# Performance work log

Measured on AMD Instinct MI355X. Metric: run time of the kernel, lower is better.

The kernel has to match this reference:

```python
import jax, jax.numpy as jnp
import numpy as np

N, E, D, H = 40000, 640000, 128, 8
DH = D // H  # out_feats per head
EPS = 1e-5


def _layernorm(x, g, b):
    mu = jnp.mean(x, axis=-1, keepdims=True)
    var = jnp.mean(jnp.square(x - mu), axis=-1, keepdims=True)
    return (x - mu) * jax.lax.rsqrt(var + EPS) * g + b


def setup_inputs() -> dict:
    key = jax.random.key(0)
    ks = jax.random.split(key, 12)
    s = 0.02
    return {
        "feat": jax.random.normal(ks[0], (N, D), dtype=jnp.float32),
        "src": jax.random.randint(ks[1], (E,), 0, N, dtype=jnp.int32),
        "dst": jax.random.randint(ks[2], (E,), 0, N, dtype=jnp.int32),
        "Wq": jax.random.normal(ks[3], (D, D), dtype=jnp.float32) * s,
        "Wk": jax.random.normal(ks[4], (D, D), dtype=jnp.float32) * s,
        "Wv": jax.random.normal(ks[5], (D, D), dtype=jnp.float32) * s,
        "ln1_g": jnp.ones((D,), jnp.float32),
        "ln1_b": jnp.zeros((D,), jnp.float32),
        "ln2_g": jnp.ones((D,), jnp.float32),
        "ln2_b": jnp.zeros((D,), jnp.float32),
        "W1": jax.random.normal(ks[6], (D, 4 * D), dtype=jnp.float32) * s,
        "b1": jnp.zeros((4 * D,), jnp.float32),
        "prelu_w": jnp.full((4 * D,), 0.25, jnp.float32),
        "W2": jax.random.normal(ks[7], (4 * D, D), dtype=jnp.float32) * s,
        "b2": jnp.zeros((D,), jnp.float32),
    }


def reference(feat, src, dst, Wq, Wk, Wv, ln1_g, ln1_b, ln2_g, ln2_b,
              W1, b1, prelu_w, W2, b2):
    n = feat.shape[0]
    feat_c = jax.lax.stop_gradient(feat)  # .clone().detach()
    q = (feat @ Wq).reshape(n, H, DH)
    k = (feat_c @ Wk).reshape(n, H, DH)
    v = (feat_c @ Wv).reshape(n, H, DH)

    # u_dot_v: per-edge, per-head dot product of k at src and q at dst
    scores = jnp.einsum('ehd,ehd->eh', k[src], q[dst]) / np.float32(np.sqrt(DH * H))

    # edge_softmax: softmax over incoming edges of each destination node
    smax = jax.ops.segment_max(scores, dst, num_segments=n)  # [N,H]
    sexp = jnp.exp(scores - smax[dst])
    ssum = jax.ops.segment_sum(sexp, dst, num_segments=n)
    a = sexp / ssum[dst]  # [E,H]  (attn_drop is eval no-op)

    # u_mul_e + sum: weighted scatter-aggregate of v[src] into dst
    msgs = v[src] * a[:, :, None]  # [E,H,DH]
    ft2 = jax.ops.segment_sum(msgs, dst, num_segments=n).reshape(n, D)

    rst = _layernorm(ft2 + feat, ln1_g, ln1_b)
    h = rst @ W1 + b1
    h = jnp.where(h >= 0, h, prelu_w * h)  # PReLU, per-channel
    ffn = h @ W2 + b2  # ffn_drop is eval no-op
    return _layernorm(rst + ffn, ln2_g, ln2_b)
```

## Files before the change

### kernel.cpp

```cpp
#include <hip/hip_runtime.h>
#include <hip/hip_bf16.h>
#include <math.h>

#define DIM 128
#define NHEAD 8
#define DHEAD 16
#define HID 512
#define LN_EPS 1e-5f
#define QSCALE 0.12751879104863297f

typedef __bf16 bf16x8 __attribute__((ext_vector_type(8)));
typedef float f32x4 __attribute__((ext_vector_type(4)));
typedef float f32x2 __attribute__((ext_vector_type(2)));
typedef _Float16 f16x2 __attribute__((ext_vector_type(2)));

__device__ inline float bf2f(unsigned int bits16) {
    return __uint_as_float(bits16 << 16);
}
__device__ inline unsigned short f2bf(float f) {
    unsigned int u = __float_as_uint(f);
    unsigned int r = u + 0x7fff + ((u >> 16) & 1);
    return (unsigned short)(r >> 16);
}
__device__ inline unsigned short f2h(float f) {
    _Float16 h = (_Float16)f;
    return __builtin_bit_cast(unsigned short, h);
}
__device__ inline float h2f(unsigned short h) {
    return (float)__builtin_bit_cast(_Float16, h);
}
__device__ inline unsigned short pk_fp8(float a, float b) {
    int r = __builtin_amdgcn_cvt_pk_fp8_f32(a, b, 0, false);
    return (unsigned short)(r & 0xffff);
}
__device__ inline f32x2 unpk_fp8_lo(unsigned int w) {
    return __builtin_amdgcn_cvt_pk_f32_fp8((int)w, false);
}
__device__ inline float fexp2(float x) { return __builtin_amdgcn_exp2f(x); }

__device__ inline void gload_lds16(const void* g, void* l) {
    __builtin_amdgcn_global_load_lds(
        (const __attribute__((address_space(1))) unsigned int*)g,
        (__attribute__((address_space(3))) unsigned int*)l, 16, 0, 0);
}

__global__ __launch_bounds__(256) void prep_count_kernel(
        int* counts, int Nn,
        const float* __restrict__ feat, unsigned short* __restrict__ featb,
        const float* __restrict__ Wq, const float* __restrict__ Wk, const float* __restrict__ Wv,
        unsigned short* __restrict__ Wqkvt,
        const float* __restrict__ W1, unsigned short* __restrict__ W1t,
        const float* __restrict__ W2, unsigned short* __restrict__ W2t,
        const int* __restrict__ dst, int E, int fb, int wb) {
    int blk = blockIdx.x, t = threadIdx.x;
    if (blk < fb) {
        int i = blk * 256 + t;
        if (i < Nn * 32) {
            float4 v = *(const float4*)(feat + (size_t)i * 4);
            ushort4 o;
            o.x = f2bf(v.x); o.y = f2bf(v.y); o.z = f2bf(v.z); o.w = f2bf(v.w);
            *(ushort4*)(featb + (size_t)i * 4) = o;
        }
    } else if (blk < wb) {
        int b2_ = blk - fb;
        if (b2_ < 192) {
            int sec = b2_ >> 6;
            const float* W = sec == 0 ? Wq : (sec == 1 ? Wk : Wv);
            int o = (b2_ & 63) * 256 + t;
            int oc = o >> 7, orow = o & 127;
            Wqkvt[sec * 16384 + o] = f2bf(W[(size_t)orow * 128 + oc]);
        } else if (b2_ < 448) {
            int o = (b2_ - 192) * 256 + t;
            int oc = o >> 7, orow = o & 127;
            W1t[o] = f2bf(W1[(size_t)orow * 512 + oc]);
        } else {
            int o = (b2_ - 448) * 256 + t;
            int oc = o >> 9, orow = o & 511;
            W2t[o] = f2bf(W2[(size_t)orow * 128 + oc]);
        }
    } else {
        int e0 = (blk - wb) * 1024 + t * 4;
        if (e0 + 3 < E) {
            int4 d = *(const int4*)(dst + e0);
            atomicAdd(&counts[d.x], 1);
            atomicAdd(&counts[d.y], 1);
            atomicAdd(&counts[d.z], 1);
            atomicAdd(&counts[d.w], 1);
        } else {
            for (int e = e0; e < E; ++e) atomicAdd(&counts[dst[e]], 1);
        }
    }
}


__global__ __launch_bounds__(256) void scanA_kernel(const int* __restrict__ counts, int* bsum, int Nn) {
    int blk = blockIdx.x, t = threadIdx.x;
    int i = blk * 1024 + t * 4;
    int s = 0;
    if (i < Nn) { int4 x = *(const int4*)(counts + i); s = x.x + x.y + x.z + x.w; }
#pragma unroll
    for (int off = 1; off < 64; off <<= 1) s += __shfl_xor(s, off, 64);
    __shared__ int wt[4];
    if ((t & 63) == 0) wt[t >> 6] = s;
    __syncthreads();
    if (t == 0) bsum[blk] = wt[0] + wt[1] + wt[2] + wt[3];
}

__global__ __launch_bounds__(256) void scanC_kernel(int* counts, const int* __restrict__ bsum,
                                                    int* offsets, int Nn, int NCH) {
    int blk = blockIdx.x, t = threadIdx.x, lane = t & 63, wv = t >> 6;
    __shared__ int wt[4];
    __shared__ int base_s;
    if (wv == 0) {
        int v = (lane < NCH) ? bsum[lane] : 0;
        int s = v;
#pragma unroll
        for (int off = 1; off < 64; off <<= 1) {
            int u = __shfl_up(s, off, 64);
            if (lane >= off) s += u;
        }
        int basev = (blk > 0) ? __shfl(s, blk - 1, 64) : 0;
        int tot = __shfl(s, NCH - 1, 64);
        if (lane == 0) {
            base_s = basev;
            if (blk == 0) offsets[Nn] = tot;
        }
    }
    int i = blk * 1024 + t * 4;
    int4 x = make_int4(0, 0, 0, 0);
    if (i < Nn) x = *(const int4*)(counts + i);
    int ts = x.x + x.y + x.z + x.w;
    int s = ts;
#pragma unroll
    for (int off = 1; off < 64; off <<= 1) {
        int u = __shfl_up(s, off, 64);
        if (lane >= off) s += u;
    }
    if (lane == 63) wt[wv] = s;
    __syncthreads();
    int woff = 0;
    for (int wi = 0; wi < wv; ++wi) woff += wt[wi];
    int excl = base_s + woff + (s - ts);
    if (i < Nn) {
        int o0 = excl, o1 = o0 + x.x, o2 = o1 + x.y, o3 = o2 + x.z;
        *(int4*)(offsets + i) = make_int4(o0, o1, o2, o3);
        *(int4*)(counts + i) = make_int4(o0, o1, o2, o3);
    }
}

#define QST 136
__global__ __launch_bounds__(256) void fill_qkv_kernel(
        const int* __restrict__ dst, const int* __restrict__ src,
        int* cursor, int* srcs, int E, int cb,
        const unsigned short* __restrict__ A, const unsigned short* __restrict__ Bt,
        unsigned short* __restrict__ qb, unsigned char* __restrict__ kv8) {
    int blk = blockIdx.x, t = threadIdx.x;
    if (blk < cb) {
        int e0 = blk * 1024 + t * 4;
        if (e0 + 3 < E) {
            int4 d = *(const int4*)(dst + e0);
            int4 sv = *(const int4*)(src + e0);
            srcs[atomicAdd(&cursor[d.x], 1)] = sv.x;
            srcs[atomicAdd(&cursor[d.y], 1)] = sv.y;
            srcs[atomicAdd(&cursor[d.z], 1)] = sv.z;
            srcs[atomicAdd(&cursor[d.w], 1)] = sv.w;
        } else {
            for (int e = e0; e < E; ++e) srcs[atomicAdd(&cursor[dst[e]], 1)] = src[e];
        }
        return;
    }
    __shared__ unsigned short smem[128 * QST];
    unsigned short* As = smem;
    unsigned short* Bs = smem + 4096;
    int q = blk - cb;
    int region = q % 3;
    int m0 = (q / 3) * 128;
    int wave = t >> 6, lane = t & 63;
    int wr = wave >> 1, wc = wave & 1;
    int lrow = lane & 15, kq = lane >> 4;
    int n0 = region * 128;
    int srow = t >> 2, scol8 = (t & 3) * 8;

    f32x4 acc[4][4] = {};
    for (int k0 = 0; k0 < 128; k0 += 32) {
        gload_lds16(A + (size_t)(m0 + srow) * 128 + k0 + scol8,      As + t * 8);
        gload_lds16(A + (size_t)(m0 + 64 + srow) * 128 + k0 + scol8, As + 2048 + t * 8);
        gload_lds16(Bt + (size_t)(n0 + srow) * 128 + k0 + scol8,      Bs + t * 8);
        gload_lds16(Bt + (size_t)(n0 + 64 + srow) * 128 + k0 + scol8, Bs + 2048 + t * 8);
        __syncthreads();
        bf16x8 af[4], bfr[4];
#pragma unroll
        for (int mi = 0; mi < 4; ++mi)
            af[mi] = *(const bf16x8*)(&As[(wr * 64 + mi * 16 + lrow) * 32 + kq * 8]);
#pragma unroll
        for (int ni = 0; ni < 4; ++ni)
            bfr[ni] = *(const bf16x8*)(&Bs[(wc * 64 + ni * 16 + lrow) * 32 + kq * 8]);
#pragma unroll
        for (int mi = 0; mi < 4; ++mi)
#pragma unroll
            for (int ni = 0; ni < 4; ++ni)
                acc[mi][ni] = __builtin_amdgcn_mfma_f32_16x16x32_bf16(af[mi], bfr[ni], acc[mi][ni], 0, 0, 0);
        __syncthreads();
    }

    float scale = (region == 0) ? QSCALE : 1.f;
#pragma unroll
    for (int ni = 0; ni < 4; ++ni) {
        int col = wc * 64 + ni * 16 + lrow;
#pragma unroll
        for (int mi = 0; mi < 4; ++mi) {
#pragma unroll
            for (int r = 0; r < 4; ++r) {
                int row = wr * 64 + mi * 16 + kq * 4 + r;
                smem[row * QST + col] = f2h(acc[mi][ni][r] * scale);
            }
        }
    }
    __syncthreads();
    if (region == 0) {
        unsigned short* outp = qb + (size_t)m0 * 128;
#pragma unroll
        for (int i = 0; i < 8; ++i) {
            int chunk = i * 256 + t;
            int row = chunk >> 4, c16 = chunk & 15;
            *(float4*)(outp + (size_t)chunk * 8) = *(const float4*)(smem + row * QST + c16 * 8);
        }
    } else {
        int half = region - 1;
#pragma unroll
        for (int i = 0; i < 4; ++i) {
            int chunk = i * 256 + t;
            int row = chunk >> 3, seg = chunk & 7;
            const unsigned short* sp = smem + row * QST + seg * 16;
            unsigned int ow[4];
#pragma unroll
            for (int j = 0; j < 4; ++j) {
                unsigned int lo = pk_fp8(h2f(sp[4 * j]), h2f(sp[4 * j + 1]));
                unsigned int hi = pk_fp8(h2f(sp[4 * j + 2]), h2f(sp[4 * j + 3]));
                ow[j] = lo | (hi << 16);
            }
            *(uint4*)(kv8 + (size_t)(m0 + row) * 256 + half * 128 + seg * 16) =
                make_uint4(ow[0], ow[1], ow[2], ow[3]);
        }
    }
}

__global__ __launch_bounds__(256) void agg_ln1_kernel(
        const unsigned short* __restrict__ qb, const unsigned short* __restrict__ kvu,
        const float* __restrict__ feat,
        const int* __restrict__ srcs, const int* __restrict__ offsets,
        const float* __restrict__ g, const float* __restrict__ b,
        unsigned short* __restrict__ rstb, int n) {
    int node = blockIdx.x * 4 + (threadIdx.x >> 6);
    int lane = threadIdx.x & 63;
    if (node >= n) return;

    unsigned int qw = ((const unsigned int*)qb)[(size_t)node * 64 + lane];
    f16x2 qp = __builtin_bit_cast(f16x2, qw);
    float q0 = (float)qp.x, q1 = (float)qp.y;

    int beg = offsets[node], end = offsets[node + 1];
    float l = 0.f, a0 = 0.f, a1 = 0.f;

    for (int idx = beg; idx < end; idx += 8) {
        int sa[8];
#pragma unroll
        for (int i = 0; i < 8; ++i) {
            int ii = idx + i;
            sa[i] = (ii < end) ? srcs[ii] : -1;
        }
        unsigned int kw[8], vw[8];
#pragma unroll
        for (int i = 0; i < 8; ++i) {
            int s = sa[i] < 0 ? 0 : sa[i];
            kw[i] = kvu[(size_t)s * 128 + lane];
        }
#pragma unroll
        for (int i = 0; i < 8; ++i) {
            int s = sa[i] < 0 ? 0 : sa[i];
            vw[i] = kvu[(size_t)s * 128 + 64 + lane];
        }
        float sc[8];
#pragma unroll
        for (int i = 0; i < 8; ++i) {
            f32x2 kk = unpk_fp8_lo(kw[i]);
            float p = fmaf(kk.x, q0, kk.y * q1);
            p += __shfl_xor(p, 1, 8);
            p += __shfl_xor(p, 2, 8);
            p += __shfl_xor(p, 4, 8);
            p = fminf(fmaxf(p, -30.f), 30.f);
            sc[i] = (sa[i] < 0) ? -1000.f : p;
        }
#pragma unroll
        for (int i = 0; i < 8; ++i) {
            float ww = fexp2(sc[i]);
            f32x2 vv = unpk_fp8_lo(vw[i]);
            l += ww;
            a0 = fmaf(vv.x, ww, a0);
            a1 = fmaf(vv.y, ww, a1);
        }
    }

    float inv = (l > 0.f) ? 1.f / l : 0.f;
    float2 fv = *(const float2*)(feat + (size_t)node * DIM + 2 * lane);
    float x0 = a0 * inv + fv.x;
    float x1 = a1 * inv + fv.y;

    float s1 = x0 + x1;
    float s2 = x0 * x0 + x1 * x1;
#pragma unroll
    for (int off = 1; off < 64; off <<= 1) {
        s1 += __shfl_xor(s1, off, 64);
        s2 += __shfl_xor(s2, off, 64);
    }
    float mean = s1 * (1.f / DIM);
    float var = s2 * (1.f / DIM) - mean * mean;
    float rinv = rsqrtf(var + LN_EPS);
    float g0 = g[2 * lane], g1 = g[2 * lane + 1];
    float b0 = b[2 * lane], b1 = b[2 * lane + 1];
    float o0 = (x0 - mean) * rinv * g0 + b0;
    float o1 = (x1 - mean) * rinv * g1 + b1;
    unsigned int packed = (unsigned int)f2bf(o0) | ((unsigned int)f2bf(o1) << 16);
    ((unsigned int*)rstb)[(size_t)node * 64 + lane] = packed;
}

__global__ __launch_bounds__(256) void ffn1_gemm(
        const unsigned short* __restrict__ A, const unsigned short* __restrict__ Bt,
        unsigned short* __restrict__ hid,
        const float* __restrict__ b1, const float* __restrict__ prelu) {
    __shared__ unsigned short smem[128 * QST];
    unsigned short* As = smem;
    unsigned short* Bs = smem + 4096;
    int t = threadIdx.x;
    int wave = t >> 6, lane = t & 63;
    int wr = wave >> 1, wc = wave & 1;
    int lrow = lane & 15, kq = lane >> 4;
    int m0 = blockIdx.y * 128;
    int n0 = blockIdx.x * 128;
    int srow = t >> 2, scol8 = (t & 3) * 8;

    f32x4 acc[4][4] = {};
    for (int k0 = 0; k0 < 128; k0 += 32) {
        gload_lds16(A + (size_t)(m0 + srow) * 128 + k0 + scol8,      As + t * 8);
        gload_lds16(A + (size_t)(m0 + 64 + srow) * 128 + k0 + scol8, As + 2048 + t * 8);
        gload_lds16(Bt + (size_t)(n0 + srow) * 128 + k0 + scol8,      Bs + t * 8);
        gload_lds16(Bt + (size_t)(n0 + 64 + srow) * 128 + k0 + scol8, Bs + 2048 + t * 8);
        __syncthreads();
        bf16x8 af[4], bfr[4];
#pragma unroll
        for (int mi = 0; mi < 4; ++mi)
            af[mi] = *(const bf16x8*)(&As[(wr * 64 + mi * 16 + lrow) * 32 + kq * 8]);
#pragma unroll
        for (int ni = 0; ni < 4; ++ni)
            bfr[ni] = *(const bf16x8*)(&Bs[(wc * 64 + ni * 16 + lrow) * 32 + kq * 8]);
#pragma unroll
        for (int mi = 0; mi < 4; ++mi)
#pragma unroll
            for (int ni = 0; ni < 4; ++ni)
                acc[mi][ni] = __builtin_amdgcn_mfma_f32_16x16x32_bf16(af[mi], bfr[ni], acc[mi][ni], 0, 0, 0);
        __syncthreads();
    }

#pragma unroll
    for (int ni = 0; ni < 4; ++ni) {
        int col = wc * 64 + ni * 16 + lrow;
        int cg = n0 + col;
        float biv = b1[cg], pwv = prelu[cg];
#pragma unroll
        for (int mi = 0; mi < 4; ++mi) {
#pragma unroll
            for (int r = 0; r < 4; ++r) {
                int row = wr * 64 + mi * 16 + kq * 4 + r;
                float v = acc[mi][ni][r] + biv;
                v = v >= 0.f ? v : pwv * v;
                smem[row * QST + col] = f2bf(v);
            }
        }
    }
    __syncthreads();
#pragma unroll
    for (int i = 0; i < 8; ++i) {
        int chunk = i * 256 + t;
        int row = chunk >> 4, c16 = chunk & 15;
        *(float4*)(hid + (size_t)(m0 + row) * 512 + n0 + c16 * 8) =
            *(const float4*)(smem + row * QST + c16 * 8);
    }
}

__global__ __launch_bounds__(256) void ffn2_ln2_kernel(
        const unsigned short* __restrict__ hid, const unsigned short* __restrict__ W2t,
        const unsigned short* __restrict__ rstb,
        const float* __restrict__ b2, const float* __restrict__ g, const float* __restrict__ bb,
        float* __restrict__ out, int Nn) {
    __shared__ unsigned short As[64 * 32];
    __shared__ unsigned short Bs[128 * 32];
    __shared__ float redS[64][4];
    __shared__ float redQ[64][4];
    int t = threadIdx.x;
    int wave = t >> 6, lane = t & 63;
    int lrow = lane & 15, kq = lane >> 4;
    int m0 = blockIdx.x * 64;
    int srow = t >> 2, scol8 = (t & 3) * 8;

    f32x4 acc[4][2] = {};
    for (int k0 = 0; k0 < 512; k0 += 32) {
        gload_lds16(hid + (size_t)(m0 + srow) * 512 + k0 + scol8, As + t * 8);
        gload_lds16(W2t + (size_t)srow * 512 + k0 + scol8,        Bs + t * 8);
        gload_lds16(W2t + (size_t)(64 + srow) * 512 + k0 + scol8, Bs + 2048 + t * 8);
        __syncthreads();
        bf16x8 af[4], bfr[2];
#pragma unroll
        for (int mi = 0; mi < 4; ++mi)
            af[mi] = *(const bf16x8*)(&As[(mi * 16 + lrow) * 32 + kq * 8]);
#pragma unroll
        for (int ni = 0; ni < 2; ++ni)
            bfr[ni] = *(const bf16x8*)(&Bs[(wave * 32 + ni * 16 + lrow) * 32 + kq * 8]);
#pragma unroll
        for (int mi = 0; mi < 4; ++mi)
#pragma unroll
            for (int ni = 0; ni < 2; ++ni)
                acc[mi][ni] = __builtin_amdgcn_mfma_f32_16x16x32_bf16(af[mi], bfr[ni], acc[mi][ni], 0, 0, 0);
        __syncthreads();
    }

    float b2v[2], gv[2], bv[2];
    int cols[2];
#pragma unroll
    for (int ni = 0; ni < 2; ++ni) {
        cols[ni] = wave * 32 + ni * 16 + lrow;
        b2v[ni] = b2[cols[ni]]; gv[ni] = g[cols[ni]]; bv[ni] = bb[cols[ni]];
    }
#pragma unroll
    for (int mi = 0; mi < 4; ++mi) {
#pragma unroll
        for (int r = 0; r < 4; ++r) {
            int rloc = mi * 16 + kq * 4 + r;
            int row = m0 + rloc;
            float ps = 0.f, pq = 0.f;
#pragma unroll
            for (int ni = 0; ni < 2; ++ni) {
                float rsv = bf2f(rstb[(size_t)row * 128 + cols[ni]]);
                float v = acc[mi][ni][r] + b2v[ni] + rsv;
                acc[mi][ni][r] = v;
                ps += v; pq += v * v;
            }
#pragma unroll
            for (int off = 1; off < 16; off <<= 1) {
                ps += __shfl_xor(ps, off, 16);
                pq += __shfl_xor(pq, off, 16);
            }
            if (lrow == 0) { redS[rloc][wave] = ps; redQ[rloc][wave] = pq; }
        }
    }
    __syncthreads();
#pragma unroll
    for (int mi = 0; mi < 4; ++mi) {
#pragma unroll
        for (int r = 0; r < 4; ++r) {
            int rloc = mi * 16 + kq * 4 + r;
            int row = m0 + rloc;
            float s1 = redS[rloc][0] + redS[rloc][1] + redS[rloc][2] + redS[rloc][3];
            float sq = redQ[rloc][0] + redQ[rloc][1] + redQ[rloc][2] + redQ[rloc][3];
            float mean = s1 * (1.f / DIM);
            float var = sq * (1.f / DIM) - mean * mean;
            float rs = rsqrtf(var + LN_EPS);
            if (row < Nn) {
#pragma unroll
                for (int ni = 0; ni < 2; ++ni)
                    out[(size_t)row * 128 + cols[ni]] =
                        (acc[mi][ni][r] - mean) * rs * gv[ni] + bv[ni];
            }
        }
    }
}


extern "C" void kernel_launch(void* const* d_in, const int* in_sizes, int n_in,
                              void* d_out, int out_size, void* d_ws, size_t ws_size,
                              hipStream_t stream) {
    const float* feat   = (const float*)d_in[0];
    const int*   src    = (const int*)d_in[1];
    const int*   dst    = (const int*)d_in[2];
    const float* Wq     = (const float*)d_in[3];
    const float* Wk     = (const float*)d_in[4];
    const float* Wv     = (const float*)d_in[5];
    const float* ln1_g  = (const float*)d_in[6];
    const float* ln1_b  = (const float*)d_in[7];
    const float* ln2_g  = (const float*)d_in[8];
    const float* ln2_b  = (const float*)d_in[9];
    const float* W1     = (const float*)d_in[10];
    const float* b1     = (const float*)d_in[11];
    const float* prelu  = (const float*)d_in[12];
    const float* W2     = (const float*)d_in[13];
    const float* b2     = (const float*)d_in[14];
    float* out = (float*)d_out;

    const int Nn = in_sizes[0] / DIM;
    const int E  = in_sizes[1];
    const int MP = (Nn + 127) & ~127;

    char* w = (char*)d_ws;
    unsigned short* qb   = (unsigned short*)w; w += (size_t)MP * DIM * 2;
    unsigned char*  kv8  = (unsigned char*)w;  w += (size_t)MP * 256;
    unsigned short* rstb = (unsigned short*)w; w += (size_t)MP * DIM * 2;
    unsigned short* featb= (unsigned short*)w; w += (size_t)MP * DIM * 2;
    unsigned short* hid  = (unsigned short*)w; w += (size_t)MP * HID * 2;
    unsigned short* Wqkvt= (unsigned short*)w; w += 3 * DIM * DIM * 2;
    unsigned short* W1t  = (unsigned short*)w; w += (size_t)HID * DIM * 2;
    unsigned short* W2t  = (unsigned short*)w; w += (size_t)DIM * HID * 2;
    int* counts  = (int*)w;  w += (size_t)Nn * 4;
    int* offsets = (int*)w;  w += (size_t)(Nn + 4) * 4;
    int* bsum    = (int*)w;  w += 64 * 4;
    int* srcs    = (int*)w;

    const int NCH = (Nn + 1023) / 1024;
    const int FB  = Nn / 8;
    const int WB  = FB + 704;
    const int CB  = (E + 1023) / 1024;

    hipMemsetAsync(counts, 0, (size_t)Nn * 4, stream);

    prep_count_kernel<<<WB + CB, 256, 0, stream>>>(
        counts, Nn, feat, featb, Wq, Wk, Wv, Wqkvt, W1, W1t, W2, W2t, dst, E, FB, WB);

    scanA_kernel<<<NCH, 256, 0, stream>>>(counts, bsum, Nn);
    scanC_kernel<<<NCH, 256, 0, stream>>>(counts, bsum, offsets, Nn, NCH);

    fill_qkv_kernel<<<CB + 3 * (MP / 128), 256, 0, stream>>>(
        dst, src, counts, srcs, E, CB, featb, Wqkvt, qb, kv8);

    agg_ln1_kernel<<<(Nn + 3) / 4, 256, 0, stream>>>(qb, (const unsigned short*)kv8, feat,
                                                     srcs, offsets, ln1_g, ln1_b, rstb, Nn);

    {
        dim3 grid(4, MP / 128);
        ffn1_gemm<<<grid, 256, 0, stream>>>(rstb, W1t, hid, b1, prelu);
    }

    ffn2_ln2_kernel<<<MP / 64, 256, 0, stream>>>(hid, W2t, rstb, b2, ln2_g, ln2_b, out, Nn);
}
```

Baseline: 258.7 us.

## Split fill and QKV GEMM kernels; restructure edge attention to lane-per-edge-head dot products

Splits the fused CSR fill and QKV GEMM kernel into two separate launches. The aggregation kernel now assigns each lane one (edge, head) pair and has it compute a full 16-element dot product from 16-byte K loads. This replaces per-lane 2-element partial products and the shuffle reductions. Attention weights are broadcast with shuffles for the V accumulation, and the fp8 conversion reads packed 32-bit words. The split loses the overlap between the fill and GEMM work, and the new loop reloads srcs for each edge in the V pass.

```diff
diff --git a/kernel.cpp b/kernel.cpp
--- a/kernel.cpp
+++ b/kernel.cpp
@@ -33,8 +33,9 @@
     int r = __builtin_amdgcn_cvt_pk_fp8_f32(a, b, 0, false);
     return (unsigned short)(r & 0xffff);
 }
-__device__ inline f32x2 unpk_fp8_lo(unsigned int w) {
-    return __builtin_amdgcn_cvt_pk_f32_fp8((int)w, false);
+template <bool HI>
+__device__ inline f32x2 unpk_fp8(unsigned int w) {
+    return __builtin_amdgcn_cvt_pk_f32_fp8((int)w, HI);
 }
 __device__ inline float fexp2(float x) { return __builtin_amdgcn_exp2f(x); }
 
@@ -148,36 +149,34 @@
     }
 }
 
+__global__ void fill_kernel(const int* __restrict__ dst, const int* __restrict__ src,
+                            int* cursor, int* srcs, int E) {
+    int e0 = (blockIdx.x * blockDim.x + threadIdx.x) * 4;
+    if (e0 + 3 < E) {
+        int4 d = *(const int4*)(dst + e0);
+        int4 sv = *(const int4*)(src + e0);
+        srcs[atomicAdd(&cursor[d.x], 1)] = sv.x;
+        srcs[atomicAdd(&cursor[d.y], 1)] = sv.y;
+        srcs[atomicAdd(&cursor[d.z], 1)] = sv.z;
+        srcs[atomicAdd(&cursor[d.w], 1)] = sv.w;
+    } else {
+        for (int e = e0; e < E; ++e) srcs[atomicAdd(&cursor[dst[e]], 1)] = src[e];
+    }
+}
+
 #define QST 136
-__global__ __launch_bounds__(256) void fill_qkv_kernel(
-        const int* __restrict__ dst, const int* __restrict__ src,
-        int* cursor, int* srcs, int E, int cb,
+__global__ __launch_bounds__(256) void qkv_gemm(
         const unsigned short* __restrict__ A, const unsigned short* __restrict__ Bt,
         unsigned short* __restrict__ qb, unsigned char* __restrict__ kv8) {
-    int blk = blockIdx.x, t = threadIdx.x;
-    if (blk < cb) {
-        int e0 = blk * 1024 + t * 4;
-        if (e0 + 3 < E) {
-            int4 d = *(const int4*)(dst + e0);
-            int4 sv = *(const int4*)(src + e0);
-            srcs[atomicAdd(&cursor[d.x], 1)] = sv.x;
-            srcs[atomicAdd(&cursor[d.y], 1)] = sv.y;
-            srcs[atomicAdd(&cursor[d.z], 1)] = sv.z;
-            srcs[atomicAdd(&cursor[d.w], 1)] = sv.w;
-        } else {
-            for (int e = e0; e < E; ++e) srcs[atomicAdd(&cursor[dst[e]], 1)] = src[e];
-        }
-        return;
-    }
     __shared__ unsigned short smem[128 * QST];
     unsigned short* As = smem;
     unsigned short* Bs = smem + 4096;
-    int q = blk - cb;
-    int region = q % 3;
-    int m0 = (q / 3) * 128;
+    int t = threadIdx.x;
     int wave = t >> 6, lane = t & 63;
     int wr = wave >> 1, wc = wave & 1;
     int lrow = lane & 15, kq = lane >> 4;
+    int m0 = blockIdx.y * 128;
+    int region = blockIdx.x;
     int n0 = region * 128;
     int srow = t >> 2, scol8 = (t & 3) * 8;
 
@@ -231,12 +230,15 @@
         for (int i = 0; i < 4; ++i) {
             int chunk = i * 256 + t;
             int row = chunk >> 3, seg = chunk & 7;
-            const unsigned short* sp = smem + row * QST + seg * 16;
+            const unsigned int* sp = (const unsigned int*)(smem + row * QST + seg * 16);
             unsigned int ow[4];
 #pragma unroll
             for (int j = 0; j < 4; ++j) {
-                unsigned int lo = pk_fp8(h2f(sp[4 * j]), h2f(sp[4 * j + 1]));
-                unsigned int hi = pk_fp8(h2f(sp[4 * j + 2]), h2f(sp[4 * j + 3]));
+                unsigned int u0 = sp[2 * j], u1 = sp[2 * j + 1];
+                unsigned int lo = pk_fp8(h2f((unsigned short)(u0 & 0xffff)),
+                                         h2f((unsigned short)(u0 >> 16)));
+                unsigned int hi = pk_fp8(h2f((unsigned short)(u1 & 0xffff)),
+                                         h2f((unsigned short)(u1 >> 16)));
                 ow[j] = lo | (hi << 16);
             }
             *(uint4*)(kv8 + (size_t)(m0 + row) * 256 + half * 128 + seg * 16) =
@@ -246,7 +248,7 @@
 }
 
 __global__ __launch_bounds__(256) void agg_ln1_kernel(
-        const unsigned short* __restrict__ qb, const unsigned short* __restrict__ kvu,
+        const unsigned short* __restrict__ qb, const unsigned char* __restrict__ kv8,
         const float* __restrict__ feat,
         const int* __restrict__ srcs, const int* __restrict__ offsets,
         const float* __restrict__ g, const float* __restrict__ b,
@@ -254,50 +256,54 @@
     int node = blockIdx.x * 4 + (threadIdx.x >> 6);
     int lane = threadIdx.x & 63;
     if (node >= n) return;
-
-    unsigned int qw = ((const unsigned int*)qb)[(size_t)node * 64 + lane];
-    f16x2 qp = __builtin_bit_cast(f16x2, qw);
-    float q0 = (float)qp.x, q1 = (float)qp.y;
+    int eo = lane >> 3;
+    int h  = lane & 7;
+
+    float qf[16];
+    {
+        uint4 qa = *(const uint4*)(qb + (size_t)node * 128 + h * 16);
+        uint4 qc = *(const uint4*)(qb + (size_t)node * 128 + h * 16 + 8);
+        unsigned int uu[8] = {qa.x, qa.y, qa.z, qa.w, qc.x, qc.y, qc.z, qc.w};
+#pragma unroll
+        for (int j = 0; j < 8; ++j) {
+            f16x2 p = __builtin_bit_cast(f16x2, uu[j]);
+            qf[2 * j] = (float)p.x; qf[2 * j + 1] = (float)p.y;
+        }
+    }
 
     int beg = offsets[node], end = offsets[node + 1];
     float l = 0.f, a0 = 0.f, a1 = 0.f;
+    const unsigned short* vtab = (const unsigned short*)kv8;
 
     for (int idx = beg; idx < end; idx += 8) {
-        int sa[8];
-#pragma unroll
-        for (int i = 0; i < 8; ++i) {
-            int ii = idx + i;
-            sa[i] = (ii < end) ? srcs[ii] : -1;
-        }
-        unsigned int kw[8], vw[8];
-#pragma unroll
-        for (int i = 0; i < 8; ++i) {
-            int s = sa[i] < 0 ? 0 : sa[i];
-            kw[i] = kvu[(size_t)s * 128 + lane];
-        }
-#pragma unroll
-        for (int i = 0; i < 8; ++i) {
-            int s = sa[i] < 0 ? 0 : sa[i];
-            vw[i] = kvu[(size_t)s * 128 + 64 + lane];
-        }
-        float sc[8];
-#pragma unroll
-        for (int i = 0; i < 8; ++i) {
-            f32x2 kk = unpk_fp8_lo(kw[i]);
-            float p = fmaf(kk.x, q0, kk.y * q1);
-            p += __shfl_xor(p, 1, 8);
-            p += __shfl_xor(p, 2, 8);
-            p += __shfl_xor(p, 4, 8);
-            p = fminf(fmaxf(p, -30.f), 30.f);
-            sc[i] = (sa[i] < 0) ? -1000.f : p;
-        }
-#pragma unroll
-        for (int i = 0; i < 8; ++i) {
-            float ww = fexp2(sc[i]);
-            f32x2 vv = unpk_fp8_lo(vw[i]);
-            l += ww;
-            a0 = fmaf(vv.x, ww, a0);
-            a1 = fmaf(vv.y, ww, a1);
+        int ie = idx + eo;
+        bool val = ie < end;
+        int smy = val ? srcs[ie] : 0;
+        uint4 kw = *(const uint4*)(kv8 + (size_t)smy * 256 + h * 16);
+        float p = 0.f;
+        {
+            f32x2 kk;
+            kk = unpk_fp8<false>(kw.x); p = fmaf(kk.x, qf[0],  p); p = fmaf(kk.y, qf[1],  p);
+            kk = unpk_fp8<true >(kw.x); p = fmaf(kk.x, qf[2],  p); p = fmaf(kk.y, qf[3],  p);
+            kk = unpk_fp8<false>(kw.y); p = fmaf(kk.x, qf[4],  p); p = fmaf(kk.y, qf[5],  p);
+            kk = unpk_fp8<true >(kw.y); p = fmaf(kk.x, qf[6],  p); p = fmaf(kk.y, qf[7],  p);
+            kk = unpk_fp8<false>(kw.z); p = fmaf(kk.x, qf[8],  p); p = fmaf(kk.y, qf[9],  p);
+            kk = unpk_fp8<true >(kw.z); p = fmaf(kk.x, qf[10], p); p = fmaf(kk.y, qf[11], p);
+            kk = unpk_fp8<false>(kw.w); p = fmaf(kk.x, qf[12], p); p = fmaf(kk.y, qf[13], p);
+            kk = unpk_fp8<true >(kw.w); p = fmaf(kk.x, qf[14], p); p = fmaf(kk.y, qf[15], p);
+        }
+        p = fminf(fmaxf(p, -30.f), 30.f);
+        float w = val ? fexp2(p) : 0.f;
+#pragma unroll
+        for (int e = 0; e < 8; ++e) {
+            int ie2 = idx + e;
+            int se = (ie2 < end) ? srcs[ie2] : 0;
+            float we = __shfl(w, e * 8 + (lane >> 3), 64);
+            unsigned int vv = vtab[(size_t)se * 128 + 64 + lane];
+            f32x2 vf = unpk_fp8<false>(vv);
+            l += we;
+            a0 = fmaf(vf.x, we, a0);
+            a1 = fmaf(vf.y, we, a1);
         }
     }
 
@@ -526,11 +532,15 @@
     scanA_kernel<<<NCH, 256, 0, stream>>>(counts, bsum, Nn);
     scanC_kernel<<<NCH, 256, 0, stream>>>(counts, bsum, offsets, Nn, NCH);
 
-    fill_qkv_kernel<<<CB + 3 * (MP / 128), 256, 0, stream>>>(
-        dst, src, counts, srcs, E, CB, featb, Wqkvt, qb, kv8);
-
-    agg_ln1_kernel<<<(Nn + 3) / 4, 256, 0, stream>>>(qb, (const unsigned short*)kv8, feat,
-                                                     srcs, offsets, ln1_g, ln1_b, rstb, Nn);
+    fill_kernel<<<CB, 256, 0, stream>>>(dst, src, counts, srcs, E);
+
+    {
+        dim3 grid(3, MP / 128);
+        qkv_gemm<<<grid, 256, 0, stream>>>(featb, Wqkvt, qb, kv8);
+    }
+
+    agg_ln1_kernel<<<(Nn + 3) / 4, 256, 0, stream>>>(qb, kv8, feat, srcs, offsets,
+                                                     ln1_g, ln1_b, rstb, Nn);
 
     {
         dim3 grid(4, MP / 128);
```

Result: slower. 279.2 us (+8.0%).
